# Kernel tuning notes

Measured on AMD Instinct MI355X. Metric: run time of the kernel, lower is better.

The kernel has to match this reference:

```python
import jax, jax.numpy as jnp
import numpy as np

B, H, N, D = 2, 16, 2048, 128

def setup_inputs() -> dict:
    key = jax.random.key(0)
    kq, kk, kv = jax.random.split(key, 3)
    q = jax.random.normal(kq, (B, H, N, D), dtype=jnp.float32)
    k = jax.random.normal(kk, (B, H, N, D), dtype=jnp.float32)
    v = jax.random.normal(kv, (B, H, N, D), dtype=jnp.float32)
    return {"q": q, "k": k, "v": v}

def reference(q, k, v):
    # scale = 1/sqrt(d) computed at forward time (scale=None in __init__)
    d = q.shape[-1]
    scale = 1.0 / jnp.sqrt(jnp.asarray(d, dtype=q.dtype))
    # scores: (B, H, N, N)
    scores = jnp.einsum('bhnd,bhmd->bhnm', q, k) * scale
    probs = jax.nn.softmax(scores, axis=-1)
    return jnp.einsum('bhnm,bhmd->bhnd', probs, v)
```

## Files before the change

kernel.cpp:

```cpp
#include <hip/hip_runtime.h>
#include <hip/hip_bf16.h>
#include <stdint.h>

#define BATCH 2
#define HEADS 16
#define BH    32
#define SEQ   2048
#define DIM   128
#define ELEMS (BATCH*HEADS*SEQ*DIM)

#define KVB   32
#define NT    (SEQ/KVB)

using f32x4  = __attribute__((ext_vector_type(4))) float;
using f32x16 = __attribute__((ext_vector_type(16))) float;
using bf16x8 = __attribute__((ext_vector_type(8))) short;
using us4    = __attribute__((ext_vector_type(4))) unsigned short;
using ui2    = __attribute__((ext_vector_type(2))) unsigned int;

__device__ __forceinline__ unsigned short f2bf(float f) {
    union { float f; uint32_t u; } v; v.f = f;
    uint32_t u = v.u;
    uint32_t r = u + 0x7FFFu + ((u >> 16) & 1u);
    return (unsigned short)(r >> 16);
}

__device__ __forceinline__ uint32_t packbf2(float lo, float hi) {
    __hip_bfloat162 h2 = __float22bfloat162_rn(make_float2(lo, hi));
    union { __hip_bfloat162 h; uint32_t u; } c; c.h = h2;
    return c.u;
}

__global__ __launch_bounds__(256) void prep(const float* __restrict__ Q,
                                            const float* __restrict__ K,
                                            const float* __restrict__ V,
                                            unsigned short* __restrict__ qb,
                                            unsigned short* __restrict__ kb,
                                            unsigned short* __restrict__ vt) {
    const int b = blockIdx.x, t = threadIdx.x;
    const float scl = 0.08838834764831845f * 1.4426950408889634f;
    if (b < 4096) {
        const bool isQ = b < 2048;
        const float* src = isQ ? Q : K;
        unsigned short* dst = isQ ? qb : kb;
        const float f = isQ ? scl : 1.0f;
        size_t base = (size_t)(isQ ? b : b - 2048) * 4096 + t * 4;
        #pragma unroll
        for (int j = 0; j < 4; ++j) {
            f32x4 v = *(const f32x4*)(src + base + j * 1024);
            us4 o;
            #pragma unroll
            for (int jj = 0; jj < 4; ++jj) o[jj] = f2bf(v[jj] * f);
            *(us4*)(dst + base + j * 1024) = o;
        }
    } else {
        __shared__ unsigned short tile[64][66];
        const int b2 = b - 4096;
        const int bh = b2 >> 6, rem = b2 & 63;
        const int n0 = (rem >> 1) * 64, d0 = (rem & 1) * 64;
        const int rr = t >> 4, cc = t & 15;
        #pragma unroll
        for (int j = 0; j < 4; ++j) {
            int row = rr + 16 * j;
            f32x4 v = *(const f32x4*)(V + ((size_t)bh * SEQ + n0 + row) * DIM + d0 + cc * 4);
            #pragma unroll
            for (int jj = 0; jj < 4; ++jj) tile[row][cc * 4 + jj] = f2bf(v[jj]);
        }
        __syncthreads();
        #pragma unroll
        for (int j = 0; j < 4; ++j) {
            int drow = rr + 16 * j;
            us4 o;
            #pragma unroll
            for (int jj = 0; jj < 4; ++jj) o[jj] = tile[cc * 4 + jj][drow];
            *(us4*)(vt + ((size_t)bh * DIM + d0 + drow) * SEQ + n0 + cc * 4) = o;
        }
    }
}

__global__ __launch_bounds__(256, 3) void attn_fwd(const unsigned short* __restrict__ Qb,
                                                   const unsigned short* __restrict__ Kb,
                                                   const unsigned short* __restrict__ VTb,
                                                   float* __restrict__ Out) {
    __shared__ __attribute__((aligned(16))) char smem[32768];

    const int bid  = blockIdx.x;
    const int xcd  = bid & 7;
    const int slot = bid >> 3;
    const int head = xcd * 4 + (slot >> 4);
    const int wid  = threadIdx.x >> 6;
    const int lane = threadIdx.x & 63;
    const int l31  = lane & 31;
    const int hL   = lane >> 5;
    const int q0   = (slot & 15) * 128 + wid * 32;

    const unsigned short* Qh = Qb + (size_t)head * SEQ * DIM;
    const char* KhB  = (const char*)(Kb  + (size_t)head * SEQ * DIM);
    const char* VThB = (const char*)(VTb + (size_t)head * DIM * SEQ);

    bf16x8 qf[8];
    {
        const char* qrow = (const char*)(Qh + (size_t)(q0 + l31) * DIM) + 16 * hL;
        #pragma unroll
        for (int u = 0; u < 8; ++u) qf[u] = *(const bf16x8*)(qrow + 32 * u);
    }

    f32x16 acc[4];
    #pragma unroll
    for (int m = 0; m < 4; ++m) acc[m] = (f32x16)(0.f);
    float m_run = -INFINITY, l_run = 0.f;

    const int swzK = (l31 & 15) << 4;

    auto STAGE = [&](int buf, int kv0) {
        #pragma unroll
        for (int i = 0; i < 2; ++i) {
            int seg = wid * 2 + i;
            int r   = seg * 4 + (lane >> 4);
            int cb  = ((lane & 15) << 4) ^ ((r & 15) << 4);
            const char* g = KhB + (((size_t)(kv0 + r)) << 8) + cb;
            __builtin_amdgcn_global_load_lds(
                (const __attribute__((address_space(1))) void*)g,
                (__attribute__((address_space(3))) void*)(smem + buf * 8192 + seg * 1024),
                16, 0, 0);
        }
        #pragma unroll
        for (int i = 0; i < 2; ++i) {
            int seg = wid * 2 + i;
            int rp  = seg * 8 + (lane >> 3);
            int c   = (lane & 7) << 4;
            int pre = c ^ ((rp & 7) << 4);
            int r   = 2 * rp + ((pre >> 6) & 1);
            int cb  = pre & 63;
            const char* g = VThB + (size_t)r * (SEQ * 2) + ((size_t)kv0 << 1) + cb;
            __builtin_amdgcn_global_load_lds(
                (const __attribute__((address_space(1))) void*)g,
                (__attribute__((address_space(3))) void*)(smem + 16384 + buf * 8192 + seg * 1024),
                16, 0, 0);
        }
    };

    STAGE(0, 0);

    #pragma unroll 1
    for (int t = 0; t < NT; ++t) {
        const int cur = t & 1;
        if (t + 1 < NT) {
            STAGE(cur ^ 1, (t + 1) * KVB);
            asm volatile("s_waitcnt vmcnt(4)" ::: "memory");
        } else {
            asm volatile("s_waitcnt vmcnt(0)" ::: "memory");
        }
        __builtin_amdgcn_s_barrier();
        asm volatile("" ::: "memory");

        const char* kb = smem + cur * 8192;
        const char* vb = smem + 16384 + cur * 8192;

        f32x16 s0 = (f32x16)(0.f);
        {
            const char* krow = kb + (size_t)l31 * 256;
            #pragma unroll
            for (int u = 0; u < 8; ++u) {
                int cb = (32 * u + 16 * hL) ^ swzK;
                bf16x8 k0 = *(const bf16x8*)(krow + cb);
                s0 = __builtin_amdgcn_mfma_f32_32x32x16_bf16(k0, qf[u], s0, 0, 0, 0);
            }
        }

        float smax = -1e30f;
        #pragma unroll
        for (int r = 0; r < 16; ++r) smax = fmaxf(smax, s0[r]);
        smax = fmaxf(smax, __shfl_xor(smax, 32));

        if (!__all(smax - m_run <= 8.f)) {
            float mnew = fmaxf(m_run, smax);
            float corr = __builtin_amdgcn_exp2f(m_run - mnew);
            #pragma unroll
            for (int m = 0; m < 4; ++m) acc[m] *= corr;
            l_run *= corr;
            m_run = mnew;
        }

        float ps[4] = {0.f, 0.f, 0.f, 0.f};
        #pragma unroll
        for (int r = 0; r < 16; ++r) {
            s0[r] = __builtin_amdgcn_exp2f(s0[r] - m_run);
            ps[r & 3] += s0[r];
        }
        l_run += (ps[0] + ps[1]) + (ps[2] + ps[3]);

        uint32_t w0[8];
        #pragma unroll
        for (int k2 = 0; k2 < 8; ++k2)
            w0[k2] = packbf2(s0[2 * k2], s0[2 * k2 + 1]);

        #pragma unroll
        for (int ss = 0; ss < 2; ++ss) {
            ui2 r02 = __builtin_amdgcn_permlane32_swap(w0[4 * ss],     w0[4 * ss + 2], false, false);
            ui2 r13 = __builtin_amdgcn_permlane32_swap(w0[4 * ss + 1], w0[4 * ss + 3], false, false);
            union { uint32_t u[4]; bf16x8 v; } Bf;
            Bf.u[0] = r02[0];
            Bf.u[1] = r13[0];
            Bf.u[2] = r02[1];
            Bf.u[3] = r13[1];
            #pragma unroll
            for (int m = 0; m < 4; ++m) {
                int rp = 16 * m + (l31 >> 1);
                int byte = ((((l31 & 1) << 6) | (32 * ss + 16 * hL)) ^ ((rp & 7) << 4));
                bf16x8 vf = *(const bf16x8*)(vb + (size_t)rp * 128 + byte);
                acc[m] = __builtin_amdgcn_mfma_f32_32x32x16_bf16(vf, Bf.v, acc[m], 0, 0, 0);
            }
        }

        asm volatile("" ::: "memory");
        __builtin_amdgcn_s_barrier();
    }

    __syncthreads();
    const float l_tot = l_run + __shfl_xor(l_run, 32);
    const float inv = 1.0f / l_tot;
    float* ob = (float*)(smem + wid * 8192);
    #pragma unroll
    for (int h = 0; h < 2; ++h) {
        #pragma unroll
        for (int mm = 0; mm < 2; ++mm) {
            int m = 2 * h + mm;
            #pragma unroll
            for (int r = 0; r < 16; ++r) {
                int dl = 32 * mm + (r & 3) + 8 * (r >> 2) + 4 * hL;
                ob[l31 * 64 + (dl ^ ((l31 & 7) << 2))] = acc[m][r] * inv;
            }
        }
        __syncthreads();
        {
            int row = lane >> 1, ch = (lane & 1) * 32;
            float* dst = Out + ((size_t)head * SEQ + q0 + row) * DIM + 64 * h + ch;
            const float* src = ob + row * 64;
            #pragma unroll
            for (int j = 0; j < 8; ++j) {
                int col = ch + 4 * j;
                *(f32x4*)(dst + 4 * j) = *(const f32x4*)(src + (col ^ ((row & 7) << 2)));
            }
        }
        if (h == 0) __syncthreads();
    }
}

extern "C" void kernel_launch(void* const* d_in, const int* in_sizes, int n_in,
                              void* d_out, int out_size, void* d_ws, size_t ws_size,
                              hipStream_t stream) {
    (void)in_sizes; (void)n_in; (void)out_size;
    const float* q = (const float*)d_in[0];
    const float* k = (const float*)d_in[1];
    const float* v = (const float*)d_in[2];
    float* out = (float*)d_out;

    const size_t needed = (size_t)ELEMS * 2 * 3;
    if (ws_size < needed) return;

    unsigned short* qb = (unsigned short*)d_ws;
    unsigned short* kb = qb + ELEMS;
    unsigned short* vt = kb + ELEMS;

    prep<<<6144, 256, 0, stream>>>(q, k, v, qb, kb, vt);
    attn_fwd<<<512, 256, 0, stream>>>(qb, kb, vt, out);
}
```

Before: 217.8 us.

## Split KV tile across wave pairs and merge partial softmax states

```diff
diff --git a/kernel.cpp b/kernel.cpp
--- a/kernel.cpp
+++ b/kernel.cpp
@@ -9,7 +9,7 @@
 #define DIM   128
 #define ELEMS (BATCH*HEADS*SEQ*DIM)
 
-#define KVB   32
+#define KVB   64
 #define NT    (SEQ/KVB)
 
 using f32x4  = __attribute__((ext_vector_type(4))) float;
@@ -78,21 +78,23 @@
     }
 }
 
-__global__ __launch_bounds__(256, 3) void attn_fwd(const unsigned short* __restrict__ Qb,
+__global__ __launch_bounds__(512, 4) void attn_fwd(const unsigned short* __restrict__ Qb,
                                                    const unsigned short* __restrict__ Kb,
                                                    const unsigned short* __restrict__ VTb,
                                                    float* __restrict__ Out) {
-    __shared__ __attribute__((aligned(16))) char smem[32768];
+    __shared__ __attribute__((aligned(16))) char smem[65536];
 
     const int bid  = blockIdx.x;
     const int xcd  = bid & 7;
     const int slot = bid >> 3;
     const int head = xcd * 4 + (slot >> 4);
     const int wid  = threadIdx.x >> 6;
+    const int qsub = wid >> 1;
+    const int h    = wid & 1;
     const int lane = threadIdx.x & 63;
     const int l31  = lane & 31;
     const int hL   = lane >> 5;
-    const int q0   = (slot & 15) * 128 + wid * 32;
+    const int q0   = (slot & 15) * 128 + qsub * 32;
 
     const unsigned short* Qh = Qb + (size_t)head * SEQ * DIM;
     const char* KhB  = (const char*)(Kb  + (size_t)head * SEQ * DIM);
@@ -111,6 +113,7 @@
     float m_run = -INFINITY, l_run = 0.f;
 
     const int swzK = (l31 & 15) << 4;
+    const int swzV = ((l31 >> 1) & 7) << 4;
 
     auto STAGE = [&](int buf, int kv0) {
         #pragma unroll
@@ -121,21 +124,21 @@
             const char* g = KhB + (((size_t)(kv0 + r)) << 8) + cb;
             __builtin_amdgcn_global_load_lds(
                 (const __attribute__((address_space(1))) void*)g,
-                (__attribute__((address_space(3))) void*)(smem + buf * 8192 + seg * 1024),
+                (__attribute__((address_space(3))) void*)(smem + buf * 16384 + seg * 1024),
                 16, 0, 0);
         }
         #pragma unroll
         for (int i = 0; i < 2; ++i) {
             int seg = wid * 2 + i;
-            int rp  = seg * 8 + (lane >> 3);
-            int c   = (lane & 7) << 4;
-            int pre = c ^ ((rp & 7) << 4);
-            int r   = 2 * rp + ((pre >> 6) & 1);
-            int cb  = pre & 63;
+            int rp  = seg * 4 + (lane >> 4);
+            int q8  = (lane & 15) << 4;
+            int pre = q8 ^ ((rp & 7) << 4);
+            int r   = 2 * rp + (pre >> 7);
+            int cb  = pre & 127;
             const char* g = VThB + (size_t)r * (SEQ * 2) + ((size_t)kv0 << 1) + cb;
             __builtin_amdgcn_global_load_lds(
                 (const __attribute__((address_space(1))) void*)g,
-                (__attribute__((address_space(3))) void*)(smem + 16384 + buf * 8192 + seg * 1024),
+                (__attribute__((address_space(3))) void*)(smem + 32768 + buf * 16384 + seg * 1024),
                 16, 0, 0);
         }
     };
@@ -154,12 +157,12 @@
         __builtin_amdgcn_s_barrier();
         asm volatile("" ::: "memory");
 
-        const char* kb = smem + cur * 8192;
-        const char* vb = smem + 16384 + cur * 8192;
+        const char* kb = smem + cur * 16384;
+        const char* vb = smem + 32768 + cur * 16384;
 
         f32x16 s0 = (f32x16)(0.f);
         {
-            const char* krow = kb + (size_t)l31 * 256;
+            const char* krow = kb + (size_t)(32 * h + l31) * 256;
             #pragma unroll
             for (int u = 0; u < 8; ++u) {
                 int cb = (32 * u + 16 * hL) ^ swzK;
@@ -204,11 +207,11 @@
             Bf.u[1] = r13[0];
             Bf.u[2] = r02[1];
             Bf.u[3] = r13[1];
+            const int cbv = (32 * (2 * h + ss) + 16 * hL) + ((l31 & 1) << 7);
             #pragma unroll
             for (int m = 0; m < 4; ++m) {
                 int rp = 16 * m + (l31 >> 1);
-                int byte = ((((l31 & 1) << 6) | (32 * ss + 16 * hL)) ^ ((rp & 7) << 4));
-                bf16x8 vf = *(const bf16x8*)(vb + (size_t)rp * 128 + byte);
+                bf16x8 vf = *(const bf16x8*)(vb + (size_t)rp * 256 + (cbv ^ swzV));
                 acc[m] = __builtin_amdgcn_mfma_f32_32x32x16_bf16(vf, Bf.v, acc[m], 0, 0, 0);
             }
         }
@@ -217,33 +220,74 @@
         __builtin_amdgcn_s_barrier();
     }
 
-    __syncthreads();
-    const float l_tot = l_run + __shfl_xor(l_run, 32);
-    const float inv = 1.0f / l_tot;
-    float* ob = (float*)(smem + wid * 8192);
-    #pragma unroll
-    for (int h = 0; h < 2; ++h) {
-        #pragma unroll
-        for (int mm = 0; mm < 2; ++mm) {
-            int m = 2 * h + mm;
+    l_run += __shfl_xor(l_run, 32);
+    __syncthreads();
+    float* mlp = (float*)smem;
+    if (h == 1) {
+        mlp[(qsub * 64 + lane) * 2]     = m_run;
+        mlp[(qsub * 64 + lane) * 2 + 1] = l_run;
+    }
+    __syncthreads();
+    float sB = 0.f;
+    if (h == 0) {
+        float mB = mlp[(qsub * 64 + lane) * 2];
+        float lB = mlp[(qsub * 64 + lane) * 2 + 1];
+        float mN = fmaxf(m_run, mB);
+        float sA = __builtin_amdgcn_exp2f(m_run - mN);
+        sB       = __builtin_amdgcn_exp2f(mB - mN);
+        l_run = sA * l_run + sB * lB;
+        #pragma unroll
+        for (int m = 0; m < 4; ++m) acc[m] *= sA;
+    }
+    __syncthreads();
+    {
+        char* accr = smem + qsub * 16384;
+        if (h == 1) {
+            #pragma unroll
+            for (int m = 0; m < 4; ++m)
+                #pragma unroll
+                for (int c = 0; c < 4; ++c) {
+                    int cidx = m * 4 + c;
+                    f32x4 v = { acc[m][4*c], acc[m][4*c+1], acc[m][4*c+2], acc[m][4*c+3] };
+                    *(f32x4*)(accr + lane * 256 + (((cidx ^ (lane & 15)) & 15) << 4)) = v;
+                }
+        }
+        __syncthreads();
+        if (h == 0) {
+            #pragma unroll
+            for (int m = 0; m < 4; ++m)
+                #pragma unroll
+                for (int c = 0; c < 4; ++c) {
+                    int cidx = m * 4 + c;
+                    f32x4 v = *(const f32x4*)(accr + lane * 256 + (((cidx ^ (lane & 15)) & 15) << 4));
+                    #pragma unroll
+                    for (int j = 0; j < 4; ++j) acc[m][4*c+j] += sB * v[j];
+                }
+        }
+    }
+    __syncthreads();
+
+    const float inv = 1.0f / l_run;
+    float* ob = (float*)(smem + qsub * 16384);
+    if (h == 0) {
+        #pragma unroll
+        for (int m = 0; m < 4; ++m) {
             #pragma unroll
             for (int r = 0; r < 16; ++r) {
-                int dl = 32 * mm + (r & 3) + 8 * (r >> 2) + 4 * hL;
-                ob[l31 * 64 + (dl ^ ((l31 & 7) << 2))] = acc[m][r] * inv;
+                int d = 32 * m + (r & 3) + 8 * (r >> 2) + 4 * hL;
+                ob[l31 * 128 + (d ^ ((l31 & 7) << 2))] = acc[m][r] * inv;
             }
         }
-        __syncthreads();
-        {
-            int row = lane >> 1, ch = (lane & 1) * 32;
-            float* dst = Out + ((size_t)head * SEQ + q0 + row) * DIM + 64 * h + ch;
-            const float* src = ob + row * 64;
-            #pragma unroll
-            for (int j = 0; j < 8; ++j) {
-                int col = ch + 4 * j;
-                *(f32x4*)(dst + 4 * j) = *(const f32x4*)(src + (col ^ ((row & 7) << 2)));
-            }
-        }
-        if (h == 0) __syncthreads();
+    }
+    __syncthreads();
+    if (h == 0) {
+        float* outp = Out + ((size_t)head * SEQ + q0) * DIM;
+        #pragma unroll
+        for (int i = 0; i < 16; ++i) {
+            int row = 2 * i + hL;
+            f32x4 v = *(const f32x4*)(ob + row * 128 + ((4 * l31) ^ ((row & 7) << 2)));
+            *(f32x4*)(outp + (size_t)row * DIM + 4 * l31) = v;
+        }
     }
 }
 
@@ -264,5 +308,5 @@
     unsigned short* vt = kb + ELEMS;
 
     prep<<<6144, 256, 0, stream>>>(q, k, v, qb, kb, vt);
-    attn_fwd<<<512, 256, 0, stream>>>(qb, kb, vt, out);
-}
+    attn_fwd<<<512, 512, 0, stream>>>(qb, kb, vt, out);
+}
```

Result: slower. 245.7 us (+12.8%).
